# Kernel tuning notes

Measured on AMD Instinct MI355X. Metric: run time of the kernel, lower is better.

The kernel has to match this reference:

```python
import jax, jax.numpy as jnp
import numpy as np

THRESHOLD = 0.0  # default threshold in forward()


def box_cxcywh_to_xyxy(b):
    cx, cy, w, h = jnp.split(b, 4, axis=-1)
    return jnp.concatenate([cx - 0.5 * w, cy - 0.5 * h, cx + 0.5 * w, cy + 0.5 * h], axis=-1)


def setup_inputs() -> dict:
    key = jax.random.key(0)
    ks = jax.random.split(key, 6)
    B, K, Q, C, A = 64, 100, 100, 82, 118
    return {
        "pred_logits": jax.random.normal(ks[0], (B, K, C), dtype=jnp.float32),
        "pred_boxes": jax.random.uniform(ks[1], (B, K, 4), dtype=jnp.float32),
        "pred_actions": jax.random.normal(ks[2], (B, Q, A), dtype=jnp.float32),
        "pred_hidx": jax.random.normal(ks[3], (B, Q, K), dtype=jnp.float32),
        "pred_oidx": jax.random.normal(ks[4], (B, Q, K), dtype=jnp.float32),
        "target_sizes": jax.random.randint(ks[5], (B, 2), 480, 1334, dtype=jnp.int32),
    }


def reference(pred_logits, pred_boxes, pred_actions, pred_hidx, pred_oidx, target_sizes):
    B, K, _ = pred_logits.shape
    # --- detection scoring / box rescale ---
    prob = jax.nn.softmax(pred_logits, axis=-1)
    scores = prob[..., :-1].max(-1)          # [B,K]
    labels = prob[..., :-1].argmax(-1)       # [B,K] int
    ts = target_sizes.astype(pred_boxes.dtype)
    img_h, img_w = ts[:, 0], ts[:, 1]
    scale = jnp.stack([img_w, img_h, img_w, img_h], axis=1)  # [B,4]
    boxes = box_cxcywh_to_xyxy(pred_boxes) * scale[:, None, :]

    # --- HOI pair scoring ---
    pair_actions = jax.nn.sigmoid(pred_actions)              # [B,Q,A]
    actions = pair_actions[..., :-1]                         # [B,Q,A-1]
    ms = 1.0 - pair_actions[..., -1]                         # matching score [B,Q]
    h_indices = jnp.argmax(pred_hidx, axis=-1)               # [B,Q] in [0,K)
    o_indices = jnp.argmax(pred_oidx, axis=-1)               # [B,Q] in [0,K)

    nseg = K * (K + 1)
    f = h_indices * (K + 1) + o_indices                      # flat (h,o) segment id [B,Q]

    def per_batch(ms_b, act_b, f_b):
        Qn = ms_b.shape[0]
        seg_max = jax.ops.segment_max(ms_b, f_b, num_segments=nseg)        # [nseg]
        cand = jnp.where(ms_b >= seg_max[f_b], jnp.arange(Qn), Qn)
        win = jax.ops.segment_min(cand, f_b, num_segments=nseg)            # [nseg]
        valid = win < Qn
        wi = jnp.minimum(win, Qn - 1)
        sorted_flat = jnp.where(valid[:, None], ms_b[wi][:, None] * act_b[wi], 0.0)  # [nseg,A-1]
        sum_flat = jax.ops.segment_sum(ms_b[:, None] * act_b, f_b, num_segments=nseg)
        return sum_flat + sorted_flat                                      # [nseg,A-1]

    flat = jax.vmap(per_batch)(ms, actions, f)               # [B,nseg,A-1]
    pair_score = flat.reshape(B, K, K + 1, -1).transpose(0, 3, 1, 2)  # [B,A-1,K,K+1]

    # boolean slicing score[:, h_inds, :][:, :, o_inds] is data-dependent; apply as mask
    h_mask = ((labels == 1) & (scores > THRESHOLD)).astype(pair_score.dtype)  # [B,K]
    o_mask = jnp.concatenate([(scores > THRESHOLD).astype(pair_score.dtype),
                              jnp.ones((B, 1), pair_score.dtype)], axis=1)    # [B,K+1]
    pair_score = pair_score * h_mask[:, None, :, None] * o_mask[:, None, None, :]
    return scores, labels, boxes, pair_score
```

## Files before the change

kernel.cpp:

```cpp
#include <hip/hip_runtime.h>
#include <cmath>

#define BB 64
#define KK 100
#define QQ 100
#define CC 82
#define AA 118
#define KP1 101
#define AM1 117
#define ROWF (KK * KP1)
#define PB 64
#define ZB 7488
#define ZCHUNK4 2525

typedef float vf4 __attribute__((ext_vector_type(4)));

__global__ __launch_bounds__(512) void fused_prep_zero(
    const float* __restrict__ logits,
    const float* __restrict__ boxes_in,
    const float* __restrict__ actions,
    const float* __restrict__ hidx,
    const float* __restrict__ oidx,
    const int*   __restrict__ tsizes,
    float* __restrict__ out_scores,
    float* __restrict__ out_labels,
    float* __restrict__ out_boxes,
    float* __restrict__ out_pair,
    int*   __restrict__ wsf,
    float* __restrict__ wsc,
    int*   __restrict__ wsl,
    int*   __restrict__ wsn)
{
    int blk = blockIdx.x;
    int tid = threadIdx.x;

    __shared__ int   sh_h[QQ], sh_o[QQ];
    __shared__ float sh_ms[QQ], sh_labf[KK];
    __shared__ int   sh_spos[KK];
    __shared__ float sh_c[QQ];
    __shared__ int   sh_wcnt[2];

    if (blk >= PB) {
        vf4* dst = ((vf4*)out_pair) + (size_t)(blk - PB) * ZCHUNK4;
        const vf4 z = {0.f, 0.f, 0.f, 0.f};
        for (int i = tid; i < ZCHUNK4; i += 512)
            dst[i] = z;
        return;
    }

    int b = blk;

    if (tid < KK) {
        const float2* l2 = (const float2*)(logits + ((size_t)b * KK + tid) * CC);
        float m = -INFINITY, best = -INFINITY; int bi = 0;
        #pragma unroll
        for (int i = 0; i < CC / 2; ++i) {
            float2 p = l2[i];
            m = fmaxf(m, fmaxf(p.x, p.y));
            if (p.x > best) { best = p.x; bi = 2 * i; }
            if (2 * i + 1 < CC - 1 && p.y > best) { best = p.y; bi = 2 * i + 1; }
        }
        float denom = 0.f;
        #pragma unroll
        for (int i = 0; i < CC / 2; ++i) {
            float2 p = l2[i];
            denom += expf(p.x - m) + expf(p.y - m);
        }
        float score = expf(best - m) / denom;
        sh_labf[tid] = (float)bi;
        sh_spos[tid] = (score > 0.0f) ? 1 : 0;
        out_scores[b * KK + tid] = score;
        out_labels[b * KK + tid] = (float)bi;

        const float4 bx = *(const float4*)(boxes_in + ((size_t)b * KK + tid) * 4);
        float ihh = (float)tsizes[b * 2 + 0];
        float iww = (float)tsizes[b * 2 + 1];
        float4 ob;
        ob.x = (bx.x - 0.5f * bx.z) * iww;
        ob.y = (bx.y - 0.5f * bx.w) * ihh;
        ob.z = (bx.x + 0.5f * bx.z) * iww;
        ob.w = (bx.y + 0.5f * bx.w) * ihh;
        *(float4*)(out_boxes + ((size_t)b * KK + tid) * 4) = ob;
    } else if (tid >= 128 && tid < 128 + QQ) {
        int q = tid - 128;
        const float4* rp = (const float4*)(hidx + ((size_t)b * QQ + q) * KK);
        float best = -INFINITY; int bi = 0;
        #pragma unroll
        for (int i = 0; i < KK / 4; ++i) {
            float4 r = rp[i];
            if (r.x > best) { best = r.x; bi = 4 * i; }
            if (r.y > best) { best = r.y; bi = 4 * i + 1; }
            if (r.z > best) { best = r.z; bi = 4 * i + 2; }
            if (r.w > best) { best = r.w; bi = 4 * i + 3; }
        }
        sh_h[q] = bi;
    } else if (tid >= 256 && tid < 256 + QQ) {
        int q = tid - 256;
        const float4* rp = (const float4*)(oidx + ((size_t)b * QQ + q) * KK);
        float best = -INFINITY; int bi = 0;
        #pragma unroll
        for (int i = 0; i < KK / 4; ++i) {
            float4 r = rp[i];
            if (r.x > best) { best = r.x; bi = 4 * i; }
            if (r.y > best) { best = r.y; bi = 4 * i + 1; }
            if (r.z > best) { best = r.z; bi = 4 * i + 2; }
            if (r.w > best) { best = r.w; bi = 4 * i + 3; }
        }
        sh_o[q] = bi;
    } else if (tid >= 384 && tid < 384 + QQ) {
        int q = tid - 384;
        float x = actions[((size_t)b * QQ + q) * AA + (AA - 1)];
        sh_ms[q] = 1.f - 1.f / (1.f + expf(-x));
    }
    __syncthreads();

    if (tid < QQ) {
        int hh = sh_h[tid], oo = sh_o[tid];
        int f = hh * KP1 + oo;
        float myms = sh_ms[tid];
        bool winf = true;
        for (int q = 0; q < QQ; ++q) {
            if (sh_h[q] * KP1 + sh_o[q] == f) {
                float m2 = sh_ms[q];
                if (m2 > myms || (m2 == myms && q < tid)) { winf = false; break; }
            }
        }
        float hm = (sh_labf[hh] == 1.0f && sh_spos[hh]) ? 1.f : 0.f;
        float om = sh_spos[oo] ? 1.f : 0.f;
        float c = myms * (winf ? 2.f : 1.f) * hm * om;
        sh_c[tid] = c;
        wsf[b * QQ + tid] = f;
        wsc[b * QQ + tid] = c;
    }
    __syncthreads();

    if (tid < 128) {
        bool flag = (tid < QQ) && (sh_c[tid] != 0.f);
        unsigned long long bal = __ballot(flag);
        if ((tid & 63) == 0) sh_wcnt[tid >> 6] = __popcll(bal);
    }
    __syncthreads();
    if (tid < 128) {
        bool flag = (tid < QQ) && (sh_c[tid] != 0.f);
        unsigned long long bal = __ballot(flag);
        int base = (tid >> 6) ? sh_wcnt[0] : 0;
        if (flag) {
            int pos = base + __popcll(bal & ((1ull << (tid & 63)) - 1ull));
            wsl[b * QQ + pos] = tid;
        }
        if (tid == 0) wsn[b] = sh_wcnt[0] + sh_wcnt[1];
    }
}

__global__ __launch_bounds__(256) void fixup_kernel(
    const float* __restrict__ actions,
    const int*   __restrict__ wsf,
    const float* __restrict__ wsc,
    const int*   __restrict__ wsl,
    const int*   __restrict__ wsn,
    float* __restrict__ out_pair)
{
    int b = blockIdx.x;
    int tid = threadIdx.x;
    int n = wsn[b];
    int total = n * AM1;
    for (int t = tid; t < total; t += 256) {
        int j = t / AM1;
        int a = t - j * AM1;
        int q = wsl[b * QQ + j];
        float c = wsc[b * QQ + q];
        int f = wsf[b * QQ + q];
        float x = actions[((size_t)b * QQ + q) * AA + a];
        float val = c / (1.f + expf(-x));
        atomicAdd(out_pair + ((size_t)(b * AM1 + a)) * ROWF + f, val);
    }
}

extern "C" void kernel_launch(void* const* d_in, const int* in_sizes, int n_in,
                              void* d_out, int out_size, void* d_ws, size_t ws_size,
                              hipStream_t stream) {
    const float* pred_logits  = (const float*)d_in[0];
    const float* pred_boxes   = (const float*)d_in[1];
    const float* pred_actions = (const float*)d_in[2];
    const float* pred_hidx    = (const float*)d_in[3];
    const float* pred_oidx    = (const float*)d_in[4];
    const int*   target_sizes = (const int*)d_in[5];

    float* out = (float*)d_out;
    float* out_scores = out;
    float* out_labels = out + BB * KK;
    float* out_boxes  = out + 2 * BB * KK;
    float* out_pair   = out + 6 * BB * KK;

    int*   wsf = (int*)d_ws;
    float* wsc = (float*)(wsf + BB * QQ);
    int*   wsl = (int*)(wsc + BB * QQ);
    int*   wsn = wsl + BB * QQ;

    fused_prep_zero<<<PB + ZB, 512, 0, stream>>>(
        pred_logits, pred_boxes, pred_actions, pred_hidx, pred_oidx,
        target_sizes, out_scores, out_labels, out_boxes, out_pair,
        wsf, wsc, wsl, wsn);

    fixup_kernel<<<BB, 256, 0, stream>>>(pred_actions, wsf, wsc, wsl, wsn,
                                         out_pair);
}
```

Before: 55.93 us.

## Move tail rows' zeroing into second kernel to overlap with fixup scatter

Splits the zero-fill of the pair-score output so the first kernel clears only the first Z1 rows. The second kernel clears the remaining rows and writes their values directly, using deduplicated per-segment sums instead of atomics. The fixup blocks for earlier rows skip rows beyond Z1. This is meant to balance work between the two launches and overlap the tail of the zeroing with the scatter, at the cost of more complex indexing and some redundant per-row scanning of the winner list.

```diff
diff --git a/kernel.cpp b/kernel.cpp
--- a/kernel.cpp
+++ b/kernel.cpp
@@ -9,8 +9,10 @@
 #define KP1 101
 #define AM1 117
 #define ROWF (KK * KP1)
+#define NROWS (BB * AM1)
 #define PB 64
-#define ZB 7488
+#define Z1 6784
+#define Z2 (NROWS - Z1)
 #define ZCHUNK4 2525
 
 typedef float vf4 __attribute__((ext_vector_type(4)));
@@ -152,7 +154,7 @@
     }
 }
 
-__global__ __launch_bounds__(256) void fixup_kernel(
+__global__ __launch_bounds__(512) void tail_kernel(
     const float* __restrict__ actions,
     const int*   __restrict__ wsf,
     const float* __restrict__ wsc,
@@ -160,13 +162,50 @@
     const int*   __restrict__ wsn,
     float* __restrict__ out_pair)
 {
-    int b = blockIdx.x;
+    int bid = blockIdx.x;
     int tid = threadIdx.x;
+
+    if (bid < Z2) {
+        int r = Z1 + bid;
+        int b = r / AM1;
+        float* row = out_pair + (size_t)r * ROWF;
+        vf4* dst = (vf4*)row;
+        const vf4 z = {0.f, 0.f, 0.f, 0.f};
+        for (int i = tid; i < ZCHUNK4; i += 512) dst[i] = z;
+        __syncthreads();
+
+        int a = r - b * AM1;
+        int n = wsn[b];
+        if (tid < n) {
+            int q = wsl[b * QQ + tid];
+            int f = wsf[b * QQ + q];
+            bool first = true;
+            for (int i = 0; i < tid; ++i) {
+                int qi = wsl[b * QQ + i];
+                if (wsf[b * QQ + qi] == f) { first = false; break; }
+            }
+            if (first) {
+                float val = 0.f;
+                for (int i = tid; i < n; ++i) {
+                    int qi = wsl[b * QQ + i];
+                    if (wsf[b * QQ + qi] == f) {
+                        float x = actions[((size_t)b * QQ + qi) * AA + a];
+                        val += wsc[b * QQ + qi] / (1.f + expf(-x));
+                    }
+                }
+                row[f] = val;
+            }
+        }
+        return;
+    }
+
+    int b = bid - Z2;
     int n = wsn[b];
     int total = n * AM1;
-    for (int t = tid; t < total; t += 256) {
+    for (int t = tid; t < total; t += 512) {
         int j = t / AM1;
         int a = t - j * AM1;
+        if (b * AM1 + a >= Z1) continue;
         int q = wsl[b * QQ + j];
         float c = wsc[b * QQ + q];
         int f = wsf[b * QQ + q];
@@ -197,11 +236,11 @@
     int*   wsl = (int*)(wsc + BB * QQ);
     int*   wsn = wsl + BB * QQ;
 
-    fused_prep_zero<<<PB + ZB, 512, 0, stream>>>(
+    fused_prep_zero<<<PB + Z1, 512, 0, stream>>>(
         pred_logits, pred_boxes, pred_actions, pred_hidx, pred_oidx,
         target_sizes, out_scores, out_labels, out_boxes, out_pair,
         wsf, wsc, wsl, wsn);
 
-    fixup_kernel<<<BB, 256, 0, stream>>>(pred_actions, wsf, wsc, wsl, wsn,
-                                         out_pair);
+    tail_kernel<<<Z2 + BB, 512, 0, stream>>>(
+        pred_actions, wsf, wsc, wsl, wsn, out_pair);
 }
```

Result: no change. 54.96 us (-1.7%).
